# Performance work log

Measured on AMD Instinct MI355X. Metric: run time of the kernel, lower is better.

## Reference

```python
import jax, jax.numpy as jnp
import numpy as np

T, B, V, HID, L = 1024, 64, 256, 512, 2


def setup_inputs() -> dict:
    key = jax.random.key(0)
    ks = jax.random.split(key, 6)
    inputs = jax.random.normal(ks[0], (T, B, V), jnp.float32)
    H = jax.random.normal(ks[1], (L, B, HID), jnp.float32) * 0.1
    s1 = 1.0 / np.sqrt(V + HID)   # torch Linear default init bound
    W_net = jax.random.uniform(ks[2], (HID, V + HID), jnp.float32, -s1, s1)
    b_net = jax.random.uniform(ks[3], (HID,), jnp.float32, -s1, s1)
    s2 = 1.0 / np.sqrt(2 * HID)
    W_deep = jax.random.uniform(ks[4], (HID, 2 * HID), jnp.float32, -s2, s2)
    b_deep = jax.random.uniform(ks[5], (HID,), jnp.float32, -s2, s2)
    return {"inputs": inputs, "H": H, "W_net": W_net, "b_net": b_net,
            "W_deep": W_deep, "b_deep": b_deep}


def _rnn_scan(xs, h0, W, b):
    # xs: [T, B, Din], h0: [B, HID]; torch does tanh(cat(x, h) @ W.T + b)
    Din = xs.shape[-1]
    Wx, Wh = W[:, :Din], W[:, Din:]  # split cat-matmul into two GEMMs (same math)
    def step(h, x):
        h = jnp.tanh(x @ Wx.T + h @ Wh.T + b)
        return h, h
    last, states = jax.lax.scan(step, h0, xs)
    return states, last  # [T, B, HID], [B, HID]


def reference(inputs, H, W_net, b_net, W_deep, b_deep):
    all_states, last = _rnn_scan(inputs, H[0], W_net, b_net)
    last_states = [last]
    for l in range(1, H.shape[0]):  # deep layers: input dim = HID
        all_states, last = _rnn_scan(all_states, H[l], W_deep, b_deep)
        last_states.append(last)
    return all_states, jnp.stack(last_states)  # [T,B,HID], [L,B,HID]
```

## Files before the change

### kernel.cpp

```cpp
#include <hip/hip_runtime.h>
#include <hip/hip_fp16.h>
#include <cstdint>
#include <cstddef>

#define TT 1024
#define BB 64
#define VV 256
#define HH 512
static const size_t TBH = (size_t)TT * BB * HH;

#define AGENT __HIP_MEMORY_SCOPE_AGENT

typedef _Float16 half2v __attribute__((ext_vector_type(2)));
union U32H2 { unsigned u; half2v h; };

__device__ __forceinline__ unsigned pack_f16x2(float a, float b) {
    __half ha = __float2half_rn(a);
    __half hb = __float2half_rn(b);
    return (unsigned)__half_as_ushort(ha) | ((unsigned)__half_as_ushort(hb) << 16);
}

__device__ __forceinline__ float tanh_fast(float x) {
    float ax = fabsf(x);
    float e = __expf(-2.0f * ax);
    float r = (1.0f - e) * __builtin_amdgcn_rcpf(1.0f + e);
    return copysignf(r, x);
}

__device__ __forceinline__ float fdot2(unsigned w, unsigned h, float acc) {
    U32H2 uw; uw.u = w;
    U32H2 uh; uh.u = h;
#if __has_builtin(__builtin_amdgcn_fdot2)
    return __builtin_amdgcn_fdot2(uw.h, uh.h, acc, false);
#else
    return acc + (float)uw.h[0] * (float)uh.h[0] + (float)uw.h[1] * (float)uh.h[1];
#endif
}

__device__ __forceinline__ int swz_us(int r) {
    int j = r >> 1;
    int js = j ^ (((j >> 5) & 7) << 2);
    return (js << 1) | (r & 1);
}

__global__ void pack_weights(const float* __restrict__ Wnet,
                             const float* __restrict__ Wdeep,
                             unsigned* __restrict__ Wq0, unsigned* __restrict__ Wq1,
                             unsigned* __restrict__ Wp0, unsigned* __restrict__ Wp1) {
    int id = blockIdx.x * 256 + threadIdx.x;
    const int NQ  = HH * (HH / 2);
    const int NP0 = (VV / 2) * HH;
    const int NP1 = (HH / 2) * HH;
    if (id < NQ) {
        int i = id >> 8, jp = id & 255;
        const float* row = Wnet + (size_t)i * (VV + HH) + VV;
        Wq0[id] = pack_f16x2(row[2 * jp], row[2 * jp + 1]);
        return;
    }
    id -= NQ;
    if (id < NQ) {
        int i = id >> 8, jp = id & 255;
        const float* row = Wdeep + (size_t)i * (2 * HH) + HH;
        Wq1[id] = pack_f16x2(row[2 * jp], row[2 * jp + 1]);
        return;
    }
    id -= NQ;
    if (id < NP0) {
        int k2 = id >> 9, n = id & 511;
        const float* row = Wnet + (size_t)n * (VV + HH);
        Wp0[id] = pack_f16x2(row[2 * k2], row[2 * k2 + 1]);
        return;
    }
    id -= NP0;
    if (id < NP1) {
        int k2 = id >> 9, n = id & 511;
        const float* row = Wdeep + (size_t)n * (2 * HH);
        Wp1[id] = pack_f16x2(row[2 * k2], row[2 * k2 + 1]);
        return;
    }
}

__device__ __forceinline__ void dot8(float* acc, unsigned a, uint4 w0, uint4 w1) {
    acc[0] = fdot2(w0.x, a, acc[0]);
    acc[1] = fdot2(w0.y, a, acc[1]);
    acc[2] = fdot2(w0.z, a, acc[2]);
    acc[3] = fdot2(w0.w, a, acc[3]);
    acc[4] = fdot2(w1.x, a, acc[4]);
    acc[5] = fdot2(w1.y, a, acc[5]);
    acc[6] = fdot2(w1.z, a, acc[6]);
    acc[7] = fdot2(w1.w, a, acc[7]);
}

__launch_bounds__(1024)
__global__ void xproj_f16(const float* __restrict__ A,
                          const unsigned* __restrict__ Wp,
                          const float* __restrict__ bias,
                          float* __restrict__ C, int K) {
    extern __shared__ unsigned As2[];
    const int m0 = blockIdx.x * 32;
    const int t = threadIdx.x;
    const int K2 = K >> 1;

    const int nf4 = 8 * K;
    const float4* Ag = (const float4*)(A + (size_t)m0 * K);
    for (int idx = t; idx < nf4; idx += 1024) {
        float4 v = Ag[idx];
        As2[idx * 2]     = pack_f16x2(v.x, v.y);
        As2[idx * 2 + 1] = pack_f16x2(v.z, v.w);
    }
    __syncthreads();

    const int rg = t >> 6;
    const int n0 = (t & 63) * 8;

    float acc0[8] = {0, 0, 0, 0, 0, 0, 0, 0};
    float acc1[8] = {0, 0, 0, 0, 0, 0, 0, 0};

    const unsigned* a0p = As2 + (size_t)(rg * 2) * K2;
    const unsigned* a1p = a0p + K2;

#pragma unroll 4
    for (int k2 = 0; k2 < K2; k2 += 2) {
        unsigned a00 = a0p[k2], a01 = a0p[k2 + 1];
        unsigned a10 = a1p[k2], a11 = a1p[k2 + 1];
        const uint4 w00 = *(const uint4*)(Wp + (size_t)k2 * 512 + n0);
        const uint4 w01 = *(const uint4*)(Wp + (size_t)k2 * 512 + n0 + 4);
        const uint4 w10 = *(const uint4*)(Wp + (size_t)(k2 + 1) * 512 + n0);
        const uint4 w11 = *(const uint4*)(Wp + (size_t)(k2 + 1) * 512 + n0 + 4);
        dot8(acc0, a00, w00, w01);
        dot8(acc1, a10, w00, w01);
        dot8(acc0, a01, w10, w11);
        dot8(acc1, a11, w10, w11);
    }

    float bv[8];
#pragma unroll
    for (int c = 0; c < 8; ++c) bv[c] = bias[n0 + c];

    float* Crow0 = C + (size_t)(m0 + rg * 2) * 512 + n0;
    float* Crow1 = Crow0 + 512;
    *(float4*)(Crow0)     = make_float4(acc0[0] + bv[0], acc0[1] + bv[1], acc0[2] + bv[2], acc0[3] + bv[3]);
    *(float4*)(Crow0 + 4) = make_float4(acc0[4] + bv[4], acc0[5] + bv[5], acc0[6] + bv[6], acc0[7] + bv[7]);
    *(float4*)(Crow1)     = make_float4(acc1[0] + bv[0], acc1[1] + bv[1], acc1[2] + bv[2], acc1[3] + bv[3]);
    *(float4*)(Crow1 + 4) = make_float4(acc1[4] + bv[4], acc1[5] + bv[5], acc1[6] + bv[6], acc1[7] + bv[7]);
}

__launch_bounds__(512, 1)
__global__ void rnn_scan4(const unsigned* __restrict__ Wq,
                          const float* __restrict__ h0,
                          float* __restrict__ states,
                          float* __restrict__ last,
                          unsigned long long* __restrict__ X) {
    __shared__ unsigned short hsh[2][512];

    const int wg = blockIdx.x;
    const int b = wg & 63;
    const int s = wg >> 6;
    const int tid = threadIdx.x;
    const int w = tid >> 6;
    const int lane = tid & 63;
    const int rowsub = lane & 7;
    const int kg = lane >> 3;
    const int rbase = s * 256 + w * 32 + rowsub;
    const bool is_fin = (kg < 4);
    const int rfin = rbase + 8 * kg;
    const int fidx = w * 32 + rowsub + 8 * kg;
    const int pidx = w * 32 + (lane & 31);
    const int rpoll = (1 - s) * 256 + pidx;

    uint4 wreg[4][8];
#pragma unroll
    for (int j = 0; j < 4; ++j) {
        const uint4* Wr = (const uint4*)(Wq + (size_t)(rbase + 8 * j) * 256 + kg * 32);
#pragma unroll
        for (int q = 0; q < 8; ++q) wreg[j][q] = Wr[q];
    }

    hsh[1][swz_us(tid)] = __half_as_ushort(__float2half_rn(h0[(size_t)b * HH + tid]));
    __syncthreads();
    uint4 hv[8];
    {
        const uint4* hb = (const uint4*)hsh[1];
#pragma unroll
        for (int q = 0; q < 8; ++q) hv[q] = hb[kg * 8 + (q ^ kg)];
    }

    unsigned long long* slotW_A = X + (((size_t)(b * 2 + s) * 2 + 0) << 8) + fidx;
    unsigned long long* slotW_B = slotW_A + 256;
    unsigned long long* slotR_A = X + (((size_t)(b * 2 + (1 - s)) * 2 + 0) << 8) + pidx;
    unsigned long long* slotR_B = slotR_A + 256;

    size_t base = (size_t)b * HH;
    const size_t tstride = (size_t)BB * HH;

    float pre_cur = 0.f;
    if (is_fin) pre_cur = states[base + rfin];

    float hlast = 0.f;
    for (int t = 0; t < TT; ++t) {
        float pre_nxt = 0.f;
        if (is_fin && t + 1 < TT) pre_nxt = states[base + tstride + rfin];

        float a0 = 0.f, a1 = 0.f, a2 = 0.f, a3 = 0.f;
#pragma unroll
        for (int q = 0; q < 8; ++q) {
            const uint4 hq = hv[q];
            a0 = fdot2(wreg[0][q].x, hq.x, a0);
            a0 = fdot2(wreg[0][q].y, hq.y, a0);
            a0 = fdot2(wreg[0][q].z, hq.z, a0);
            a0 = fdot2(wreg[0][q].w, hq.w, a0);
            a1 = fdot2(wreg[1][q].x, hq.x, a1);
            a1 = fdot2(wreg[1][q].y, hq.y, a1);
            a1 = fdot2(wreg[1][q].z, hq.z, a1);
            a1 = fdot2(wreg[1][q].w, hq.w, a1);
            a2 = fdot2(wreg[2][q].x, hq.x, a2);
            a2 = fdot2(wreg[2][q].y, hq.y, a2);
            a2 = fdot2(wreg[2][q].z, hq.z, a2);
            a2 = fdot2(wreg[2][q].w, hq.w, a2);
            a3 = fdot2(wreg[3][q].x, hq.x, a3);
            a3 = fdot2(wreg[3][q].y, hq.y, a3);
            a3 = fdot2(wreg[3][q].z, hq.z, a3);
            a3 = fdot2(wreg[3][q].w, hq.w, a3);
        }
        a0 += __shfl_xor(a0, 8);  a0 += __shfl_xor(a0, 16);  a0 += __shfl_xor(a0, 32);
        a1 += __shfl_xor(a1, 8);  a1 += __shfl_xor(a1, 16);  a1 += __shfl_xor(a1, 32);
        a2 += __shfl_xor(a2, 8);  a2 += __shfl_xor(a2, 16);  a2 += __shfl_xor(a2, 32);
        a3 += __shfl_xor(a3, 8);  a3 += __shfl_xor(a3, 16);  a3 += __shfl_xor(a3, 32);

        const int p = t & 1;
        if (is_fin) {
            float af = (kg == 0) ? a0 : (kg == 1) ? a1 : (kg == 2) ? a2 : a3;
            float h = tanh_fast(pre_cur + af);
            hlast = h;
            states[base + rfin] = h;
            unsigned long long msg = ((unsigned long long)(unsigned)(t + 1) << 32)
                                   | (unsigned long long)__float_as_uint(h);
            __hip_atomic_store(p ? slotW_B : slotW_A, msg, __ATOMIC_RELAXED, AGENT);
            hsh[p][swz_us(rfin)] = __half_as_ushort(__float2half_rn(h));
        } else {
            unsigned long long* slot = p ? slotR_B : slotR_A;
            unsigned long long v;
            do {
                v = __hip_atomic_load(slot, __ATOMIC_RELAXED, AGENT);
            } while ((unsigned)(v >> 32) != (unsigned)(t + 1));
            float hp_ = __uint_as_float((unsigned)v);
            hsh[p][swz_us(rpoll)] = __half_as_ushort(__float2half_rn(hp_));
        }
        __syncthreads();

        const uint4* hb = (const uint4*)hsh[p];
#pragma unroll
        for (int q = 0; q < 8; ++q) hv[q] = hb[kg * 8 + (q ^ kg)];

        pre_cur = pre_nxt;
        base += tstride;
    }

    if (is_fin) last[(size_t)b * HH + rfin] = hlast;
}

extern "C" void kernel_launch(void* const* d_in, const int* in_sizes, int n_in,
                              void* d_out, int out_size, void* d_ws, size_t ws_size,
                              hipStream_t stream) {
    (void)in_sizes; (void)n_in; (void)out_size; (void)ws_size;
    const float* inputs = (const float*)d_in[0];
    const float* H      = (const float*)d_in[1];
    const float* Wnet   = (const float*)d_in[2];
    const float* bnet   = (const float*)d_in[3];
    const float* Wdeep  = (const float*)d_in[4];
    const float* bdeep  = (const float*)d_in[5];
    float* out = (float*)d_out;

    unsigned long long* X = (unsigned long long*)d_ws;
    unsigned* Wq0 = (unsigned*)(X + 64 * 2 * 2 * 256);
    unsigned* Wq1 = Wq0 + HH * (HH / 2);
    unsigned* Wp0 = Wq1 + HH * (HH / 2);
    unsigned* Wp1 = Wp0 + (VV / 2) * HH;

    hipLaunchKernelGGL(pack_weights, dim3(1792), dim3(256), 0, stream,
                       Wnet, Wdeep, Wq0, Wq1, Wp0, Wp1);

    hipLaunchKernelGGL(xproj_f16, dim3((TT * BB) / 32), dim3(1024),
                       32 * (VV / 2) * sizeof(unsigned), stream,
                       inputs, Wp0, bnet, out, VV);

    hipLaunchKernelGGL(rnn_scan4, dim3(128), dim3(512), 0, stream,
                       Wq0, H, out, out + TBH, X);

    hipLaunchKernelGGL(xproj_f16, dim3((TT * BB) / 32), dim3(1024),
                       32 * (HH / 2) * sizeof(unsigned), stream,
                       out, Wp1, bdeep, out, HH);

    hipLaunchKernelGGL(rnn_scan4, dim3(128), dim3(512), 0, stream,
                       Wq1, H + (size_t)BB * HH, out, out + TBH + (size_t)BB * HH, X);
}
```

Baseline: 4.253 ms.

## Run each batch's recurrence in one workgroup with LDS-resident weight slice

Adds a scan kernel that processes a whole batch element in a single 512-thread workgroup. Six eighths of the f16 recurrent weight matrix stay in registers and the remaining two eighths go into 128KB of dynamic LDS. This replaces the two-workgroup scheme, which exchanged half of each hidden state per step through global-memory atomic polling, with a local __syncthreads. The cross-lane reduction now uses DPP and permlane swaps. In exchange each thread does twice the dot-product work per step plus extra LDS weight reads, and the launch falls back to the old kernel if the large LDS allocation is refused.

```diff
diff --git a/kernel.cpp b/kernel.cpp
--- a/kernel.cpp
+++ b/kernel.cpp
@@ -41,6 +41,24 @@
     int j = r >> 1;
     int js = j ^ (((j >> 5) & 7) << 2);
     return (js << 1) | (r & 1);
+}
+
+__device__ __forceinline__ float bsum8(float v) {
+    int d = __builtin_amdgcn_update_dpp(0, __float_as_int(v), 0x128, 0xF, 0xF, true);
+    v += __int_as_float(d);
+#if __has_builtin(__builtin_amdgcn_permlane16_swap) && __has_builtin(__builtin_amdgcn_permlane32_swap)
+    {
+        auto r1 = __builtin_amdgcn_permlane16_swap(__float_as_uint(v), __float_as_uint(v), false, false);
+        v = __uint_as_float(r1[0]) + __uint_as_float(r1[1]);
+        auto r2 = __builtin_amdgcn_permlane32_swap(__float_as_uint(v), __float_as_uint(v), false, false);
+        v = __uint_as_float(r2[0]) + __uint_as_float(r2[1]);
+    }
+#else
+    int l = (int)(threadIdx.x & 63);
+    v += __int_as_float(__builtin_amdgcn_ds_bpermute((l ^ 16) << 2, __float_as_int(v)));
+    v += __int_as_float(__builtin_amdgcn_ds_bpermute((l ^ 32) << 2, __float_as_int(v)));
+#endif
+    return v;
 }
 
 __global__ void pack_weights(const float* __restrict__ Wnet,
@@ -143,6 +161,123 @@
     *(float4*)(Crow0 + 4) = make_float4(acc0[4] + bv[4], acc0[5] + bv[5], acc0[6] + bv[6], acc0[7] + bv[7]);
     *(float4*)(Crow1)     = make_float4(acc1[0] + bv[0], acc1[1] + bv[1], acc1[2] + bv[2], acc1[3] + bv[3]);
     *(float4*)(Crow1 + 4) = make_float4(acc1[4] + bv[4], acc1[5] + bv[5], acc1[6] + bv[6], acc1[7] + bv[7]);
+}
+
+#define SMEM_SCAN_BYTES (128 * 1024 + 2 * HH * 2)
+
+__launch_bounds__(512, 2)
+__global__ void rnn_scan5(const unsigned* __restrict__ Wq,
+                          const float* __restrict__ h0,
+                          float* __restrict__ states,
+                          float* __restrict__ last) {
+    extern __shared__ char smem[];
+    uint4* Wl = (uint4*)smem;
+    unsigned short* hsh0 = (unsigned short*)(smem + 128 * 1024);
+    unsigned short* hsh1 = hsh0 + HH;
+
+    const int b = blockIdx.x;
+    const int tid = threadIdx.x;
+    const int w = tid >> 6;
+    const int lane = tid & 63;
+    const int rowsub = lane & 7;
+    const int kg = lane >> 3;
+    const int rfin = w * 64 + rowsub + 8 * kg;
+
+    uint4 wreg[6][8];
+#pragma unroll
+    for (int j = 0; j < 6; ++j) {
+        const uint4* Wr = (const uint4*)(Wq + (size_t)(w * 64 + rowsub + 8 * j) * 256) + kg * 8;
+#pragma unroll
+        for (int q = 0; q < 8; ++q) wreg[j][q] = Wr[q];
+    }
+#pragma unroll
+    for (int j = 6; j < 8; ++j) {
+        const uint4* Wr = (const uint4*)(Wq + (size_t)(w * 64 + rowsub + 8 * j) * 256) + kg * 8;
+        const int rowLocal = w * 16 + (j - 6) * 8 + rowsub;
+#pragma unroll
+        for (int q = 0; q < 8; ++q)
+            Wl[rowLocal * 64 + kg * 8 + (q ^ rowsub)] = Wr[q];
+    }
+
+    hsh1[swz_us(tid)] = __half_as_ushort(__float2half_rn(h0[(size_t)b * HH + tid]));
+    __syncthreads();
+
+    const uint4* wbase = Wl + ((size_t)(w * 16 + rowsub) * 64 + kg * 8);
+    const int hoff = kg * 8;
+    const int wswz = swz_us(rfin);
+
+    size_t base = (size_t)b * HH;
+    const size_t tstride = (size_t)BB * HH;
+    float pre_cur = states[base + rfin];
+    float h = 0.f;
+
+    const uint4* hbA = (const uint4*)hsh1;
+    const uint4* hbB = (const uint4*)hsh0;
+
+    auto step = [&](const uint4* __restrict__ hbr, unsigned short* __restrict__ hshw, int t) {
+        float pre_nxt = 0.f;
+        if (t + 1 < TT) pre_nxt = states[base + tstride + rfin];
+
+        float a0 = 0.f, a1 = 0.f, a2 = 0.f, a3 = 0.f;
+        float a4 = 0.f, a5 = 0.f, a6 = 0.f, a7 = 0.f;
+#pragma unroll
+        for (int q = 0; q < 8; ++q) {
+            const uint4 hq = hbr[hoff + (q ^ kg)];
+            const uint4 w6 = wbase[(q ^ rowsub)];
+            const uint4 w7 = wbase[(q ^ rowsub) + 512];
+            a0 = fdot2(wreg[0][q].x, hq.x, a0);
+            a0 = fdot2(wreg[0][q].y, hq.y, a0);
+            a0 = fdot2(wreg[0][q].z, hq.z, a0);
+            a0 = fdot2(wreg[0][q].w, hq.w, a0);
+            a1 = fdot2(wreg[1][q].x, hq.x, a1);
+            a1 = fdot2(wreg[1][q].y, hq.y, a1);
+            a1 = fdot2(wreg[1][q].z, hq.z, a1);
+            a1 = fdot2(wreg[1][q].w, hq.w, a1);
+            a2 = fdot2(wreg[2][q].x, hq.x, a2);
+            a2 = fdot2(wreg[2][q].y, hq.y, a2);
+            a2 = fdot2(wreg[2][q].z, hq.z, a2);
+            a2 = fdot2(wreg[2][q].w, hq.w, a2);
+            a3 = fdot2(wreg[3][q].x, hq.x, a3);
+            a3 = fdot2(wreg[3][q].y, hq.y, a3);
+            a3 = fdot2(wreg[3][q].z, hq.z, a3);
+            a3 = fdot2(wreg[3][q].w, hq.w, a3);
+            a4 = fdot2(wreg[4][q].x, hq.x, a4);
+            a4 = fdot2(wreg[4][q].y, hq.y, a4);
+            a4 = fdot2(wreg[4][q].z, hq.z, a4);
+            a4 = fdot2(wreg[4][q].w, hq.w, a4);
+            a5 = fdot2(wreg[5][q].x, hq.x, a5);
+            a5 = fdot2(wreg[5][q].y, hq.y, a5);
+            a5 = fdot2(wreg[5][q].z, hq.z, a5);
+            a5 = fdot2(wreg[5][q].w, hq.w, a5);
+            a6 = fdot2(w6.x, hq.x, a6);
+            a6 = fdot2(w6.y, hq.y, a6);
+            a6 = fdot2(w6.z, hq.z, a6);
+            a6 = fdot2(w6.w, hq.w, a6);
+            a7 = fdot2(w7.x, hq.x, a7);
+            a7 = fdot2(w7.y, hq.y, a7);
+            a7 = fdot2(w7.z, hq.z, a7);
+            a7 = fdot2(w7.w, hq.w, a7);
+        }
+        a0 = bsum8(a0); a1 = bsum8(a1); a2 = bsum8(a2); a3 = bsum8(a3);
+        a4 = bsum8(a4); a5 = bsum8(a5); a6 = bsum8(a6); a7 = bsum8(a7);
+
+        float af = (kg == 0) ? a0 : (kg == 1) ? a1 : (kg == 2) ? a2 : (kg == 3) ? a3
+                 : (kg == 4) ? a4 : (kg == 5) ? a5 : (kg == 6) ? a6 : a7;
+        h = tanh_fast(pre_cur + af);
+        states[base + rfin] = h;
+        hshw[wswz] = __half_as_ushort(__float2half_rn(h));
+        __syncthreads();
+
+        pre_cur = pre_nxt;
+        base += tstride;
+    };
+
+    for (int t = 0; t < TT; t += 2) {
+        step(hbA, hsh0, t);
+        step(hbB, hsh1, t + 1);
+    }
+
+    last[(size_t)b * HH + rfin] = h;
 }
 
 __launch_bounds__(512, 1)
@@ -230,13 +365,13 @@
         const int p = t & 1;
         if (is_fin) {
             float af = (kg == 0) ? a0 : (kg == 1) ? a1 : (kg == 2) ? a2 : a3;
-            float h = tanh_fast(pre_cur + af);
-            hlast = h;
-            states[base + rfin] = h;
+            float hh = tanh_fast(pre_cur + af);
+            hlast = hh;
+            states[base + rfin] = hh;
             unsigned long long msg = ((unsigned long long)(unsigned)(t + 1) << 32)
-                                   | (unsigned long long)__float_as_uint(h);
+                                   | (unsigned long long)__float_as_uint(hh);
             __hip_atomic_store(p ? slotW_B : slotW_A, msg, __ATOMIC_RELAXED, AGENT);
-            hsh[p][swz_us(rfin)] = __half_as_ushort(__float2half_rn(h));
+            hsh[p][swz_us(rfin)] = __half_as_ushort(__float2half_rn(hh));
         } else {
             unsigned long long* slot = p ? slotR_B : slotR_A;
             unsigned long long v;
@@ -277,6 +412,17 @@
     unsigned* Wp0 = Wq1 + HH * (HH / 2);
     unsigned* Wp1 = Wp0 + (VV / 2) * HH;
 
+    static int scan5_ok = -1;
+    if (scan5_ok < 0) {
+        hipError_t e1 = hipFuncSetAttribute((const void*)rnn_scan5,
+                                            hipFuncAttributeMaxDynamicSharedMemorySize,
+                                            SMEM_SCAN_BYTES);
+        hipFuncAttributes fa;
+        hipError_t e2 = hipFuncGetAttributes(&fa, (const void*)rnn_scan5);
+        scan5_ok = (e1 == hipSuccess && e2 == hipSuccess &&
+                    fa.maxDynamicSharedSizeBytes >= (int)SMEM_SCAN_BYTES) ? 1 : 0;
+    }
+
     hipLaunchKernelGGL(pack_weights, dim3(1792), dim3(256), 0, stream,
                        Wnet, Wdeep, Wq0, Wq1, Wp0, Wp1);
 
@@ -284,13 +430,23 @@
                        32 * (VV / 2) * sizeof(unsigned), stream,
                        inputs, Wp0, bnet, out, VV);
 
-    hipLaunchKernelGGL(rnn_scan4, dim3(128), dim3(512), 0, stream,
-                       Wq0, H, out, out + TBH, X);
+    if (scan5_ok) {
+        hipLaunchKernelGGL(rnn_scan5, dim3(64), dim3(512), SMEM_SCAN_BYTES, stream,
+                           Wq0, H, out, out + TBH);
+    } else {
+        hipLaunchKernelGGL(rnn_scan4, dim3(128), dim3(512), 0, stream,
+                           Wq0, H, out, out + TBH, X);
+    }
 
     hipLaunchKernelGGL(xproj_f16, dim3((TT * BB) / 32), dim3(1024),
                        32 * (HH / 2) * sizeof(unsigned), stream,
                        out, Wp1, bdeep, out, HH);
 
-    hipLaunchKernelGGL(rnn_scan4, dim3(128), dim3(512), 0, stream,
-                       Wq1, H + (size_t)BB * HH, out, out + TBH + (size_t)BB * HH, X);
-}
+    if (scan5_ok) {
+        hipLaunchKernelGGL(rnn_scan5, dim3(64), dim3(512), SMEM_SCAN_BYTES, stream,
+                           Wq1, H + (size_t)BB * HH, out, out + TBH + (size_t)BB * HH);
+    } else {
+        hipLaunchKernelGGL(rnn_scan4, dim3(128), dim3(512), 0, stream,
+                           Wq1, H + (size_t)BB * HH, out, out + TBH + (size_t)BB * HH, X);
+    }
+}
```

Result: faster. 4.160 ms (-2.2%).

## Run each batch row's recurrence in one workgroup, removing cross-workgroup polling

Applied to the files above, without the earlier changes.

The recurrent scan kernel now gives each batch element a single 512-thread workgroup that owns all 512 hidden rows, where before two workgroups per batch element swapped half-states through global-memory atomics and spin polling. Six of the eight weight row-groups stay in registers and the other two are streamed from global or cache each step with software prefetch. Cross-lane reductions move to DPP/permlane swaps, and the barrier is a raw s_barrier with a manual waitcnt on double-buffered shared memory. This removes the inter-workgroup handshake latency but halves the number of workgroups, doubles per-thread math, and adds weight reloads every timestep.

```diff
diff --git a/kernel.cpp b/kernel.cpp
--- a/kernel.cpp
+++ b/kernel.cpp
@@ -8,8 +8,6 @@
 #define VV 256
 #define HH 512
 static const size_t TBH = (size_t)TT * BB * HH;
-
-#define AGENT __HIP_MEMORY_SCOPE_AGENT
 
 typedef _Float16 half2v __attribute__((ext_vector_type(2)));
 union U32H2 { unsigned u; half2v h; };
@@ -41,6 +39,24 @@
     int j = r >> 1;
     int js = j ^ (((j >> 5) & 7) << 2);
     return (js << 1) | (r & 1);
+}
+
+__device__ __forceinline__ float bsum8(float v) {
+    int d = __builtin_amdgcn_update_dpp(0, __float_as_int(v), 0x128, 0xF, 0xF, true);
+    v += __int_as_float(d);
+#if __has_builtin(__builtin_amdgcn_permlane16_swap) && __has_builtin(__builtin_amdgcn_permlane32_swap)
+    {
+        auto r1 = __builtin_amdgcn_permlane16_swap(__float_as_uint(v), __float_as_uint(v), false, false);
+        v = __uint_as_float(r1[0]) + __uint_as_float(r1[1]);
+        auto r2 = __builtin_amdgcn_permlane32_swap(__float_as_uint(v), __float_as_uint(v), false, false);
+        v = __uint_as_float(r2[0]) + __uint_as_float(r2[1]);
+    }
+#else
+    int l = (int)(threadIdx.x & 63);
+    v += __int_as_float(__builtin_amdgcn_ds_bpermute((l ^ 16) << 2, __float_as_int(v)));
+    v += __int_as_float(__builtin_amdgcn_ds_bpermute((l ^ 32) << 2, __float_as_int(v)));
+#endif
+    return v;
 }
 
 __global__ void pack_weights(const float* __restrict__ Wnet,
@@ -146,65 +162,63 @@
 }
 
 __launch_bounds__(512, 1)
-__global__ void rnn_scan4(const unsigned* __restrict__ Wq,
+__global__ void rnn_scan8(const unsigned* __restrict__ Wq,
                           const float* __restrict__ h0,
                           float* __restrict__ states,
-                          float* __restrict__ last,
-                          unsigned long long* __restrict__ X) {
-    __shared__ unsigned short hsh[2][512];
-
-    const int wg = blockIdx.x;
-    const int b = wg & 63;
-    const int s = wg >> 6;
+                          float* __restrict__ last) {
+    __shared__ unsigned short hsh0[HH];
+    __shared__ unsigned short hsh1[HH];
+
+    const int b = blockIdx.x;
     const int tid = threadIdx.x;
     const int w = tid >> 6;
     const int lane = tid & 63;
     const int rowsub = lane & 7;
     const int kg = lane >> 3;
-    const int rbase = s * 256 + w * 32 + rowsub;
-    const bool is_fin = (kg < 4);
-    const int rfin = rbase + 8 * kg;
-    const int fidx = w * 32 + rowsub + 8 * kg;
-    const int pidx = w * 32 + (lane & 31);
-    const int rpoll = (1 - s) * 256 + pidx;
-
-    uint4 wreg[4][8];
+    const int rfin = w * 64 + rowsub + 8 * kg;
+
+    uint4 wreg[6][8];
 #pragma unroll
-    for (int j = 0; j < 4; ++j) {
-        const uint4* Wr = (const uint4*)(Wq + (size_t)(rbase + 8 * j) * 256 + kg * 32);
+    for (int j = 0; j < 6; ++j) {
+        const uint4* Wr = (const uint4*)(Wq + (size_t)(w * 64 + rowsub + 8 * j) * 256) + kg * 8;
 #pragma unroll
         for (int q = 0; q < 8; ++q) wreg[j][q] = Wr[q];
     }
-
-    hsh[1][swz_us(tid)] = __half_as_ushort(__float2half_rn(h0[(size_t)b * HH + tid]));
+    const uint4* g6 = (const uint4*)(Wq + (size_t)(w * 64 + rowsub + 48) * 256) + kg * 8;
+    const uint4* g7 = (const uint4*)(Wq + (size_t)(w * 64 + rowsub + 56) * 256) + kg * 8;
+
+    hsh1[swz_us(tid)] = __half_as_ushort(__float2half_rn(h0[(size_t)b * HH + tid]));
     __syncthreads();
-    uint4 hv[8];
-    {
-        const uint4* hb = (const uint4*)hsh[1];
-#pragma unroll
-        for (int q = 0; q < 8; ++q) hv[q] = hb[kg * 8 + (q ^ kg)];
-    }
-
-    unsigned long long* slotW_A = X + (((size_t)(b * 2 + s) * 2 + 0) << 8) + fidx;
-    unsigned long long* slotW_B = slotW_A + 256;
-    unsigned long long* slotR_A = X + (((size_t)(b * 2 + (1 - s)) * 2 + 0) << 8) + pidx;
-    unsigned long long* slotR_B = slotR_A + 256;
+
+    const int hoff = kg * 8;
+    const int wswz = swz_us(rfin);
 
     size_t base = (size_t)b * HH;
     const size_t tstride = (size_t)BB * HH;
-
-    float pre_cur = 0.f;
-    if (is_fin) pre_cur = states[base + rfin];
-
-    float hlast = 0.f;
-    for (int t = 0; t < TT; ++t) {
+    float pre_cur = states[base + rfin];
+    float h = 0.f;
+
+    const uint4* hbA = (const uint4*)hsh1;
+    const uint4* hbB = (const uint4*)hsh0;
+
+    auto step = [&](const uint4* __restrict__ hbr, unsigned short* __restrict__ hshw, int t) {
         float pre_nxt = 0.f;
-        if (is_fin && t + 1 < TT) pre_nxt = states[base + tstride + rfin];
+        if (t + 1 < TT) pre_nxt = states[base + tstride + rfin];
+
+        uint4 hq = hbr[hoff + (0 ^ kg)];
+        uint4 w6 = g6[0];
+        uint4 w7 = g7[0];
 
         float a0 = 0.f, a1 = 0.f, a2 = 0.f, a3 = 0.f;
+        float a4 = 0.f, a5 = 0.f, a6 = 0.f, a7 = 0.f;
 #pragma unroll
         for (int q = 0; q < 8; ++q) {
-            const uint4 hq = hv[q];
+            uint4 hq_n, w6_n, w7_n;
+            if (q < 7) {
+                hq_n = hbr[hoff + ((q + 1) ^ kg)];
+                w6_n = g6[q + 1];
+                w7_n = g7[q + 1];
+            }
             a0 = fdot2(wreg[0][q].x, hq.x, a0);
             a0 = fdot2(wreg[0][q].y, hq.y, a0);
             a0 = fdot2(wreg[0][q].z, hq.z, a0);
@@ -221,42 +235,47 @@
             a3 = fdot2(wreg[3][q].y, hq.y, a3);
             a3 = fdot2(wreg[3][q].z, hq.z, a3);
             a3 = fdot2(wreg[3][q].w, hq.w, a3);
+            a4 = fdot2(wreg[4][q].x, hq.x, a4);
+            a4 = fdot2(wreg[4][q].y, hq.y, a4);
+            a4 = fdot2(wreg[4][q].z, hq.z, a4);
+            a4 = fdot2(wreg[4][q].w, hq.w, a4);
+            a5 = fdot2(wreg[5][q].x, hq.x, a5);
+            a5 = fdot2(wreg[5][q].y, hq.y, a5);
+            a5 = fdot2(wreg[5][q].z, hq.z, a5);
+            a5 = fdot2(wreg[5][q].w, hq.w, a5);
+            a6 = fdot2(w6.x, hq.x, a6);
+            a6 = fdot2(w6.y, hq.y, a6);
+            a6 = fdot2(w6.z, hq.z, a6);
+            a6 = fdot2(w6.w, hq.w, a6);
+            a7 = fdot2(w7.x, hq.x, a7);
+            a7 = fdot2(w7.y, hq.y, a7);
+            a7 = fdot2(w7.z, hq.z, a7);
+            a7 = fdot2(w7.w, hq.w, a7);
+            if (q < 7) { hq = hq_n; w6 = w6_n; w7 = w7_n; }
         }
-        a0 += __shfl_xor(a0, 8);  a0 += __shfl_xor(a0, 16);  a0 += __shfl_xor(a0, 32);
-        a1 += __shfl_xor(a1, 8);  a1 += __shfl_xor(a1, 16);  a1 += __shfl_xor(a1, 32);
-        a2 += __shfl_xor(a2, 8);  a2 += __shfl_xor(a2, 16);  a2 += __shfl_xor(a2, 32);
-        a3 += __shfl_xor(a3, 8);  a3 += __shfl_xor(a3, 16);  a3 += __shfl_xor(a3, 32);
-
-        const int p = t & 1;
-        if (is_fin) {
-            float af = (kg == 0) ? a0 : (kg == 1) ? a1 : (kg == 2) ? a2 : a3;
-            float h = tanh_fast(pre_cur + af);
-            hlast = h;
-            states[base + rfin] = h;
-            unsigned long long msg = ((unsigned long long)(unsigned)(t + 1) << 32)
-                                   | (unsigned long long)__float_as_uint(h);
-            __hip_atomic_store(p ? slotW_B : slotW_A, msg, __ATOMIC_RELAXED, AGENT);
-            hsh[p][swz_us(rfin)] = __half_as_ushort(__float2half_rn(h));
-        } else {
-            unsigned long long* slot = p ? slotR_B : slotR_A;
-            unsigned long long v;
-            do {
-                v = __hip_atomic_load(slot, __ATOMIC_RELAXED, AGENT);
-            } while ((unsigned)(v >> 32) != (unsigned)(t + 1));
-            float hp_ = __uint_as_float((unsigned)v);
-            hsh[p][swz_us(rpoll)] = __half_as_ushort(__float2half_rn(hp_));
-        }
-        __syncthreads();
-
-        const uint4* hb = (const uint4*)hsh[p];
-#pragma unroll
-        for (int q = 0; q < 8; ++q) hv[q] = hb[kg * 8 + (q ^ kg)];
+        a0 = bsum8(a0); a1 = bsum8(a1); a2 = bsum8(a2); a3 = bsum8(a3);
+        a4 = bsum8(a4); a5 = bsum8(a5); a6 = bsum8(a6); a7 = bsum8(a7);
+
+        float af = (kg == 0) ? a0 : (kg == 1) ? a1 : (kg == 2) ? a2 : (kg == 3) ? a3
+                 : (kg == 4) ? a4 : (kg == 5) ? a5 : (kg == 6) ? a6 : a7;
+        h = tanh_fast(pre_cur + af);
+        states[base + rfin] = h;
+        hshw[wswz] = __half_as_ushort(__float2half_rn(h));
+
+        asm volatile("s_waitcnt lgkmcnt(0)" ::: "memory");
+        __builtin_amdgcn_s_barrier();
+        __builtin_amdgcn_sched_barrier(0);
 
         pre_cur = pre_nxt;
         base += tstride;
-    }
-
-    if (is_fin) last[(size_t)b * HH + rfin] = hlast;
+    };
+
+    for (int t = 0; t < TT; t += 2) {
+        step(hbA, hsh0, t);
+        step(hbB, hsh1, t + 1);
+    }
+
+    last[(size_t)b * HH + rfin] = h;
 }
 
 extern "C" void kernel_launch(void* const* d_in, const int* in_sizes, int n_in,
@@ -271,8 +290,7 @@
     const float* bdeep  = (const float*)d_in[5];
     float* out = (float*)d_out;
 
-    unsigned long long* X = (unsigned long long*)d_ws;
-    unsigned* Wq0 = (unsigned*)(X + 64 * 2 * 2 * 256);
+    unsigned* Wq0 = (unsigned*)d_ws;
     unsigned* Wq1 = Wq0 + HH * (HH / 2);
     unsigned* Wp0 = Wq1 + HH * (HH / 2);
     unsigned* Wp1 = Wp0 + (VV / 2) * HH;
@@ -284,13 +302,13 @@
                        32 * (VV / 2) * sizeof(unsigned), stream,
                        inputs, Wp0, bnet, out, VV);
 
-    hipLaunchKernelGGL(rnn_scan4, dim3(128), dim3(512), 0, stream,
-                       Wq0, H, out, out + TBH, X);
+    hipLaunchKernelGGL(rnn_scan8, dim3(64), dim3(512), 0, stream,
+                       Wq0, H, out, out + TBH);
 
     hipLaunchKernelGGL(xproj_f16, dim3((TT * BB) / 32), dim3(1024),
                        32 * (HH / 2) * sizeof(unsigned), stream,
                        out, Wp1, bdeep, out, HH);
 
-    hipLaunchKernelGGL(rnn_scan4, dim3(128), dim3(512), 0, stream,
-                       Wq1, H + (size_t)BB * HH, out, out + TBH + (size_t)BB * HH, X);
-}
+    hipLaunchKernelGGL(rnn_scan8, dim3(64), dim3(512), 0, stream,
+                       Wq1, H + (size_t)BB * HH, out, out + TBH + (size_t)BB * HH);
+}
```

After: 6.574 ms. 54.6% more time.

## Split recurrent scan across four workgroups per batch with DPP reductions

Applied to the files above, without the earlier changes.

The recurrent scan now spreads each batch row's 512 hidden units over four workgroups instead of two, so each thread keeps half as many weight registers and the grid grows to 256 blocks. Each block publishes its 128 results and polls three peers through flag-tagged global slots. The cross-lane reduction switches from shuffles to DPP and permlane swaps, and the loop is unrolled by two with ping-pong shared buffers and a raw barrier. The aim is less per-step dot-product work and shorter reductions, at the cost of more cross-workgroup polling traffic, more dependency on other blocks, and a requirement that all 256 blocks be co-resident.

```diff
diff --git a/kernel.cpp b/kernel.cpp
--- a/kernel.cpp
+++ b/kernel.cpp
@@ -41,6 +41,24 @@
     int j = r >> 1;
     int js = j ^ (((j >> 5) & 7) << 2);
     return (js << 1) | (r & 1);
+}
+
+__device__ __forceinline__ float bsum8(float v) {
+    int d = __builtin_amdgcn_update_dpp(0, __float_as_int(v), 0x128, 0xF, 0xF, true);
+    v += __int_as_float(d);
+#if __has_builtin(__builtin_amdgcn_permlane16_swap) && __has_builtin(__builtin_amdgcn_permlane32_swap)
+    {
+        auto r1 = __builtin_amdgcn_permlane16_swap(__float_as_uint(v), __float_as_uint(v), false, false);
+        v = __uint_as_float(r1[0]) + __uint_as_float(r1[1]);
+        auto r2 = __builtin_amdgcn_permlane32_swap(__float_as_uint(v), __float_as_uint(v), false, false);
+        v = __uint_as_float(r2[0]) + __uint_as_float(r2[1]);
+    }
+#else
+    int l = (int)(threadIdx.x & 63);
+    v += __int_as_float(__builtin_amdgcn_ds_bpermute((l ^ 16) << 2, __float_as_int(v)));
+    v += __int_as_float(__builtin_amdgcn_ds_bpermute((l ^ 32) << 2, __float_as_int(v)));
+#endif
+    return v;
 }
 
 __global__ void pack_weights(const float* __restrict__ Wnet,
@@ -146,12 +164,13 @@
 }
 
 __launch_bounds__(512, 1)
-__global__ void rnn_scan4(const unsigned* __restrict__ Wq,
+__global__ void rnn_scan9(const unsigned* __restrict__ Wq,
                           const float* __restrict__ h0,
                           float* __restrict__ states,
                           float* __restrict__ last,
                           unsigned long long* __restrict__ X) {
-    __shared__ unsigned short hsh[2][512];
+    __shared__ unsigned short hshA[HH];
+    __shared__ unsigned short hshB[HH];
 
     const int wg = blockIdx.x;
     const int b = wg & 63;
@@ -161,102 +180,96 @@
     const int lane = tid & 63;
     const int rowsub = lane & 7;
     const int kg = lane >> 3;
-    const int rbase = s * 256 + w * 32 + rowsub;
-    const bool is_fin = (kg < 4);
-    const int rfin = rbase + 8 * kg;
-    const int fidx = w * 32 + rowsub + 8 * kg;
-    const int pidx = w * 32 + (lane & 31);
-    const int rpoll = (1 - s) * 256 + pidx;
-
-    uint4 wreg[4][8];
+
+    const int r0 = s * 128 + w * 16 + rowsub;
+
+    const bool is_fin = (kg < 2);
+    const int rf = s * 128 + w * 16 + (lane & 15);
+    const int fslot = w * 16 + (lane & 15);
+
+    const bool is_poll = (tid < 384);
+    const int qq = (s + 1 + (tid >> 7)) & 3;
+    const int fr = tid & 127;
+    const int hrow = qq * 128 + fr;
+
+    uint4 wreg[2][8];
 #pragma unroll
-    for (int j = 0; j < 4; ++j) {
-        const uint4* Wr = (const uint4*)(Wq + (size_t)(rbase + 8 * j) * 256 + kg * 32);
+    for (int j = 0; j < 2; ++j) {
+        const uint4* Wr = (const uint4*)(Wq + (size_t)(r0 + 8 * j) * 256) + kg * 8;
 #pragma unroll
         for (int q = 0; q < 8; ++q) wreg[j][q] = Wr[q];
     }
 
-    hsh[1][swz_us(tid)] = __half_as_ushort(__float2half_rn(h0[(size_t)b * HH + tid]));
+    unsigned long long* wrA   = X + ((((size_t)b * 4 + s)  * 2 + 0) << 7) + fslot;
+    unsigned long long* wrB   = wrA + 128;
+    unsigned long long* pollA = X + ((((size_t)b * 4 + qq) * 2 + 0) << 7) + fr;
+    unsigned long long* pollB = pollA + 128;
+
+    hshA[swz_us(tid)] = __half_as_ushort(__float2half_rn(h0[(size_t)b * HH + tid]));
     __syncthreads();
-    uint4 hv[8];
-    {
-        const uint4* hb = (const uint4*)hsh[1];
-#pragma unroll
-        for (int q = 0; q < 8; ++q) hv[q] = hb[kg * 8 + (q ^ kg)];
-    }
-
-    unsigned long long* slotW_A = X + (((size_t)(b * 2 + s) * 2 + 0) << 8) + fidx;
-    unsigned long long* slotW_B = slotW_A + 256;
-    unsigned long long* slotR_A = X + (((size_t)(b * 2 + (1 - s)) * 2 + 0) << 8) + pidx;
-    unsigned long long* slotR_B = slotR_A + 256;
 
     size_t base = (size_t)b * HH;
     const size_t tstride = (size_t)BB * HH;
-
     float pre_cur = 0.f;
-    if (is_fin) pre_cur = states[base + rfin];
-
-    float hlast = 0.f;
-    for (int t = 0; t < TT; ++t) {
+    if (is_fin) pre_cur = states[base + rf];
+    float h = 0.f;
+
+    auto step = [&](const unsigned short* __restrict__ hbr,
+                    unsigned short* __restrict__ hshw, int t) {
         float pre_nxt = 0.f;
-        if (is_fin && t + 1 < TT) pre_nxt = states[base + tstride + rfin];
-
-        float a0 = 0.f, a1 = 0.f, a2 = 0.f, a3 = 0.f;
+        if (is_fin && t + 1 < TT) pre_nxt = states[base + tstride + rf];
+
+        const uint4* hb = (const uint4*)hbr;
+        float a0 = 0.f, a1 = 0.f, c0 = 0.f, c1 = 0.f;
 #pragma unroll
         for (int q = 0; q < 8; ++q) {
-            const uint4 hq = hv[q];
+            const uint4 hq = hb[kg * 8 + (q ^ kg)];
             a0 = fdot2(wreg[0][q].x, hq.x, a0);
-            a0 = fdot2(wreg[0][q].y, hq.y, a0);
+            a1 = fdot2(wreg[0][q].y, hq.y, a1);
             a0 = fdot2(wreg[0][q].z, hq.z, a0);
-            a0 = fdot2(wreg[0][q].w, hq.w, a0);
-            a1 = fdot2(wreg[1][q].x, hq.x, a1);
-            a1 = fdot2(wreg[1][q].y, hq.y, a1);
-            a1 = fdot2(wreg[1][q].z, hq.z, a1);
-            a1 = fdot2(wreg[1][q].w, hq.w, a1);
-            a2 = fdot2(wreg[2][q].x, hq.x, a2);
-            a2 = fdot2(wreg[2][q].y, hq.y, a2);
-            a2 = fdot2(wreg[2][q].z, hq.z, a2);
-            a2 = fdot2(wreg[2][q].w, hq.w, a2);
-            a3 = fdot2(wreg[3][q].x, hq.x, a3);
-            a3 = fdot2(wreg[3][q].y, hq.y, a3);
-            a3 = fdot2(wreg[3][q].z, hq.z, a3);
-            a3 = fdot2(wreg[3][q].w, hq.w, a3);
+            a1 = fdot2(wreg[0][q].w, hq.w, a1);
+            c0 = fdot2(wreg[1][q].x, hq.x, c0);
+            c1 = fdot2(wreg[1][q].y, hq.y, c1);
+            c0 = fdot2(wreg[1][q].z, hq.z, c0);
+            c1 = fdot2(wreg[1][q].w, hq.w, c1);
         }
-        a0 += __shfl_xor(a0, 8);  a0 += __shfl_xor(a0, 16);  a0 += __shfl_xor(a0, 32);
-        a1 += __shfl_xor(a1, 8);  a1 += __shfl_xor(a1, 16);  a1 += __shfl_xor(a1, 32);
-        a2 += __shfl_xor(a2, 8);  a2 += __shfl_xor(a2, 16);  a2 += __shfl_xor(a2, 32);
-        a3 += __shfl_xor(a3, 8);  a3 += __shfl_xor(a3, 16);  a3 += __shfl_xor(a3, 32);
+        float ra = bsum8(a0 + a1);
+        float rc = bsum8(c0 + c1);
 
         const int p = t & 1;
         if (is_fin) {
-            float af = (kg == 0) ? a0 : (kg == 1) ? a1 : (kg == 2) ? a2 : a3;
-            float h = tanh_fast(pre_cur + af);
-            hlast = h;
-            states[base + rfin] = h;
+            float af = (kg == 0) ? ra : rc;
+            h = tanh_fast(pre_cur + af);
+            states[base + rf] = h;
             unsigned long long msg = ((unsigned long long)(unsigned)(t + 1) << 32)
                                    | (unsigned long long)__float_as_uint(h);
-            __hip_atomic_store(p ? slotW_B : slotW_A, msg, __ATOMIC_RELAXED, AGENT);
-            hsh[p][swz_us(rfin)] = __half_as_ushort(__float2half_rn(h));
-        } else {
-            unsigned long long* slot = p ? slotR_B : slotR_A;
+            __hip_atomic_store(p ? wrB : wrA, msg, __ATOMIC_RELAXED, AGENT);
+            hshw[swz_us(rf)] = __half_as_ushort(__float2half_rn(h));
+        }
+        if (is_poll) {
+            unsigned long long* slot = p ? pollB : pollA;
             unsigned long long v;
             do {
                 v = __hip_atomic_load(slot, __ATOMIC_RELAXED, AGENT);
             } while ((unsigned)(v >> 32) != (unsigned)(t + 1));
-            float hp_ = __uint_as_float((unsigned)v);
-            hsh[p][swz_us(rpoll)] = __half_as_ushort(__float2half_rn(hp_));
+            hshw[swz_us(hrow)] =
+                __half_as_ushort(__float2half_rn(__uint_as_float((unsigned)v)));
         }
-        __syncthreads();
-
-        const uint4* hb = (const uint4*)hsh[p];
-#pragma unroll
-        for (int q = 0; q < 8; ++q) hv[q] = hb[kg * 8 + (q ^ kg)];
+
+        asm volatile("s_waitcnt lgkmcnt(0)" ::: "memory");
+        __builtin_amdgcn_s_barrier();
+        __builtin_amdgcn_sched_barrier(0);
 
         pre_cur = pre_nxt;
         base += tstride;
-    }
-
-    if (is_fin) last[(size_t)b * HH + rfin] = hlast;
+    };
+
+    for (int t = 0; t < TT; t += 2) {
+        step(hshA, hshB, t);
+        step(hshB, hshA, t + 1);
+    }
+
+    if (is_fin) last[(size_t)b * HH + rf] = h;
 }
 
 extern "C" void kernel_launch(void* const* d_in, const int* in_sizes, int n_in,
@@ -272,7 +285,7 @@
     float* out = (float*)d_out;
 
     unsigned long long* X = (unsigned long long*)d_ws;
-    unsigned* Wq0 = (unsigned*)(X + 64 * 2 * 2 * 256);
+    unsigned* Wq0 = (unsigned*)(X + 64 * 4 * 2 * 128);
     unsigned* Wq1 = Wq0 + HH * (HH / 2);
     unsigned* Wp0 = Wq1 + HH * (HH / 2);
     unsigned* Wp1 = Wp0 + (VV / 2) * HH;
@@ -284,13 +297,13 @@
                        32 * (VV / 2) * sizeof(unsigned), stream,
                        inputs, Wp0, bnet, out, VV);
 
-    hipLaunchKernelGGL(rnn_scan4, dim3(128), dim3(512), 0, stream,
+    hipLaunchKernelGGL(rnn_scan9, dim3(256), dim3(512), 0, stream,
                        Wq0, H, out, out + TBH, X);
 
     hipLaunchKernelGGL(xproj_f16, dim3((TT * BB) / 32), dim3(1024),
                        32 * (HH / 2) * sizeof(unsigned), stream,
                        out, Wp1, bdeep, out, HH);
 
-    hipLaunchKernelGGL(rnn_scan4, dim3(128), dim3(512), 0, stream,
+    hipLaunchKernelGGL(rnn_scan9, dim3(256), dim3(512), 0, stream,
                        Wq1, H + (size_t)BB * HH, out, out + TBH + (size_t)BB * HH, X);
 }
```

New measurement: 4.184 ms. No clear change (-1.6%).
